# Kernel optimization log

Hardware: AMD Instinct MI355X
Metric: run time of the kernel (lower is better)

Reference implementation:

```python
import jax, jax.numpy as jnp
import numpy as np

N_NODES = 100000
N_EDGES = 1600000
IN_CH = 128
HIDDEN = 64
N_CLASSES = 40


def setup_inputs() -> dict:
    key = jax.random.key(0)
    k_x, k_e, k_w1, k_w2 = jax.random.split(key, 4)
    x = jax.random.normal(k_x, (N_NODES, IN_CH), dtype=jnp.float32)
    edge_index = jax.random.randint(k_e, (2, N_EDGES), 0, N_NODES, dtype=jnp.int64)
    # Glorot-style init for GCN weights
    W1 = jax.random.normal(k_w1, (IN_CH, HIDDEN), dtype=jnp.float32) * (1.0 / np.sqrt(IN_CH))
    b1 = jnp.zeros((HIDDEN,), dtype=jnp.float32)
    W2 = jax.random.normal(k_w2, (HIDDEN, N_CLASSES), dtype=jnp.float32) * (1.0 / np.sqrt(HIDDEN))
    b2 = jnp.zeros((N_CLASSES,), dtype=jnp.float32)
    return {"x": x, "edge_index": edge_index, "W1": W1, "b1": b1, "W2": W2, "b2": b2}


def reference(x, edge_index, W1, b1, W2, b2):
    n = x.shape[0]
    # PyG GCNConv: add self-loops, symmetric degree normalization
    loop = jnp.arange(n, dtype=edge_index.dtype)
    src = jnp.concatenate([edge_index[0], loop])  # message sources j
    dst = jnp.concatenate([edge_index[1], loop])  # aggregation targets i
    w = jnp.ones(src.shape[0], dtype=x.dtype)     # edge_weight=None -> ones
    deg = jax.ops.segment_sum(w, dst, num_segments=n)
    dinv = jnp.where(deg > 0, jax.lax.rsqrt(jnp.maximum(deg, 1e-12)), 0.0)
    norm = dinv[src] * dinv[dst]                  # [E+N]

    def gcn_conv(h, W, b):
        hw = h @ W                                # transform first (fewer flops)
        msg = hw[src] * norm[:, None]             # gather + normalize
        return jax.ops.segment_sum(msg, dst, num_segments=n) + b  # scatter-add

    h = jax.nn.relu(gcn_conv(x, W1, b1))
    # dropout is identity in eval mode
    out = gcn_conv(h, W2, b2)
    return out
```

## Files before the change

### kernel.cpp

```cpp
#include <hip/hip_runtime.h>
#include <hip/hip_bf16.h>

#define NNODES 100000
#define NEDGES 1600000
#define IN_CH 128
#define HID 64
#define NC 40
#define NPAD 100352
#define NBUK 196
#define CAP 9216
#define BCHUNK 4096
#define NBIN 391
#define HW2S 64

typedef unsigned short ushort_t;
typedef unsigned int uint_t;
typedef __attribute__((ext_vector_type(8))) short short8;
typedef __attribute__((ext_vector_type(4))) float floatx4;

__device__ __forceinline__ ushort_t f2bf(float f) {
    union { float ff; unsigned int i; } t;
    t.ff = f;
    unsigned int r = t.i + 0x7fff + ((t.i >> 16) & 1);
    return (ushort_t)(r >> 16);
}
__device__ __forceinline__ float2 unpk(uint_t p) {
    union { unsigned int i; float f; } a, b;
    a.i = p << 16;
    b.i = p & 0xffff0000u;
    return make_float2(a.f, b.f);
}
__device__ __forceinline__ void acc2(float2& a, uint_t p) {
    union { unsigned int i; float f; } lo, hi;
    lo.i = p << 16;
    hi.i = p & 0xffff0000u;
    a.x += lo.f;
    a.y += hi.f;
}

__global__ __launch_bounds__(256) void k_init(
    const float* __restrict__ W1, ushort_t* __restrict__ Wp,
    int* __restrict__ gcur, ushort_t* __restrict__ hw2, int n)
{
    int b = blockIdx.x, t = threadIdx.x;
    if (b < 32) {
        int i = b * 256 + t;
        int j = i & 7;
        int m = (i >> 3) & 15;
        int ct = (i >> 7) & 3;
        int quad = (i >> 9) & 3;
        int kc = i >> 11;
        int k = kc * 32 + quad * 8 + j;
        int c = ct * 16 + m;
        Wp[i] = f2bf(W1[k * HID + c]);
    } else {
        if (t < NBUK) gcur[t] = t * CAP;
        if (t >= 224 && t < 224 + NC) hw2[(size_t)n * HW2S + (t - 224)] = 0;
    }
}

__global__ __launch_bounds__(256) void k_bin0(
    const int* __restrict__ srcs, const int* __restrict__ dsts,
    int* __restrict__ gcur, uint_t* __restrict__ tmp, int e)
{
    __shared__ uint_t pk[BCHUNK];
    __shared__ ushort_t bk[BCHUNK];
    __shared__ int hist[NBUK];
    __shared__ int base[NBUK];
    int t = threadIdx.x;
    int begin = blockIdx.x * BCHUNK;
    int cnt = e - begin; if (cnt > BCHUNK) cnt = BCHUNK;

    for (int i = t; i < NBUK; i += 256) hist[i] = 0;
    __syncthreads();
    for (int j = t; j < cnt; j += 256) {
        int d = dsts[begin + j];
        int s = srcs[begin + j];
        int b = d >> 9;
        pk[j] = (uint_t)s | ((uint_t)(d & 511) << 17);
        bk[j] = (ushort_t)b;
        atomicAdd(&hist[b], 1);
    }
    __syncthreads();
    for (int i = t; i < NBUK; i += 256) {
        base[i] = atomicAdd(&gcur[i], hist[i]);
        hist[i] = 0;
    }
    __syncthreads();
    for (int j = t; j < cnt; j += 256) {
        int b = bk[j];
        int r = atomicAdd(&hist[b], 1);
        int pos = base[b] + r;
        if (pos < (b + 1) * CAP) tmp[pos] = pk[j];
    }
}

__global__ __launch_bounds__(256) void k_sort(
    const uint_t* __restrict__ tmp, const int* __restrict__ gcur,
    int* __restrict__ row_start, float* __restrict__ dinv,
    uint_t* __restrict__ es, int n, int e)
{
    __shared__ int cnt[512];
    __shared__ int sc[512];
    __shared__ int red[256];
    int t = threadIdx.x;
    int b = blockIdx.x;
    int d0 = b << 9;
    int total = gcur[b] - b * CAP;
    if (total > CAP) total = CAP;
    int part = 0;
    for (int i = t; i < b; i += 256) part += gcur[i] - i * CAP;
    red[t] = part;
    cnt[t] = 0; cnt[t + 256] = 0;
    __syncthreads();
    for (int off = 128; off > 0; off >>= 1) {
        if (t < off) red[t] += red[t + off];
        __syncthreads();
    }
    int gb = red[0];
    const uint_t* seg = tmp + b * CAP;
    for (int j = t; j < total; j += 256)
        atomicAdd(&cnt[seg[j] >> 17], 1);
    __syncthreads();
    sc[t] = cnt[t]; sc[t + 256] = cnt[t + 256];
    __syncthreads();
    for (int off = 1; off < 512; off <<= 1) {
        int v0 = (t >= off) ? sc[t - off] : 0;
        int i1 = t + 256;
        int v1 = (i1 >= off) ? sc[i1 - off] : 0;
        __syncthreads();
        sc[t] += v0; sc[i1] += v1;
        __syncthreads();
    }
#pragma unroll
    for (int q = 0; q < 2; ++q) {
        int i = t + q * 256;
        int node = d0 + i;
        int start = gb + sc[i] - cnt[i];
        if (node < n) {
            row_start[node] = start;
            dinv[node] = rsqrtf((float)cnt[i] + 1.0f);
        }
        cnt[i] = start;
    }
    __syncthreads();
    for (int j = t; j < total; j += 256) {
        uint_t p = seg[j];
        int ld = (int)(p >> 17);
        int pos = atomicAdd(&cnt[ld], 1);
        es[pos] = p & 0x1FFFFu;
    }
    if (b == NBUK - 1 && t == 0) row_start[n] = e;
}

__global__ __launch_bounds__(256) void k_gemm1(
    const float* __restrict__ x, const ushort_t* __restrict__ Wp,
    const float* __restrict__ dinv, ushort_t* __restrict__ hw1, int n)
{
    int wave = threadIdx.x >> 6;
    int lane = threadIdx.x & 63;
    int m = lane & 15;
    int quad = lane >> 4;
    int row = blockIdx.x * 64 + wave * 16 + m;
    int rowc = row < n ? row : (n - 1);
    const float* xr = x + (size_t)rowc * IN_CH + quad * 8;

    floatx4 acc[4];
#pragma unroll
    for (int ct = 0; ct < 4; ++ct) acc[ct] = (floatx4){0.f, 0.f, 0.f, 0.f};

#pragma unroll
    for (int kc = 0; kc < 4; ++kc) {
        float4 xa = *(const float4*)(xr + kc * 32);
        float4 xb = *(const float4*)(xr + kc * 32 + 4);
        short8 a;
        a[0] = (short)f2bf(xa.x); a[1] = (short)f2bf(xa.y);
        a[2] = (short)f2bf(xa.z); a[3] = (short)f2bf(xa.w);
        a[4] = (short)f2bf(xb.x); a[5] = (short)f2bf(xb.y);
        a[6] = (short)f2bf(xb.z); a[7] = (short)f2bf(xb.w);
#pragma unroll
        for (int ct = 0; ct < 4; ++ct) {
            short8 b = *(const short8*)(Wp + ((((kc * 4 + quad) * 4 + ct) * 16 + m) << 3));
            acc[ct] = __builtin_amdgcn_mfma_f32_16x16x32_bf16(a, b, acc[ct], 0, 0, 0);
        }
    }
    int r0 = blockIdx.x * 64 + wave * 16 + quad * 4;
#pragma unroll
    for (int r = 0; r < 4; ++r) {
        int rr = r0 + r;
        if (rr < n) {
            float di = dinv[rr];
            ushort_t* o = hw1 + (size_t)rr * HID + m;
#pragma unroll
            for (int ct = 0; ct < 4; ++ct) o[ct * 16] = f2bf(acc[ct][r] * di);
        } else if (rr == n) {
            ushort_t* o = hw1 + (size_t)n * HID + m;
#pragma unroll
            for (int ct = 0; ct < 4; ++ct) o[ct * 16] = 0;
        }
    }
}

__global__ __launch_bounds__(256) void k_agg1(
    const int* __restrict__ row_start, const uint_t* __restrict__ es,
    const float* __restrict__ dinv, const uint_t* __restrict__ hw1u,
    const float* __restrict__ b1, const float* __restrict__ W2,
    ushort_t* __restrict__ hw2, int n)
{
    __shared__ float wsm[HID * NC];
    __shared__ float hsm[32][68];
    for (int i = threadIdx.x; i < HID * NC; i += 256) wsm[i] = W2[i];
    __syncthreads();

    int lane = threadIdx.x & 63;
    int obase = lane & 56;
    int ol = lane & 7;
    int slot = threadIdx.x >> 3;
    int node = blockIdx.x * 32 + slot;
    bool valid = node < n;
    int rs = valid ? row_start[node] : 0;
    int re = valid ? row_start[node + 1] : 0;
    float di = valid ? dinv[node] : 0.f;
    int selfrow = valid ? node : n;

    float2 c0, c1, c2, c3;
    {
        uint4 sp = *(const uint4*)(hw1u + (size_t)selfrow * 32 + ol * 4);
        c0 = unpk(sp.x); c1 = unpk(sp.y); c2 = unpk(sp.z); c3 = unpk(sp.w);
    }
    for (int base = rs; base < re; base += 16) {
        int i0 = base + ol, i1 = base + 8 + ol;
        int elA = (i0 < re) ? (int)es[i0] : n;
        int elB = (i1 < re) ? (int)es[i1] : n;
        int nw = re - base;
        uint4 pA[8], pB[8];
#pragma unroll
        for (int b = 0; b < 8; ++b) {
            int s = __shfl(elA, obase + b);
            pA[b] = *(const uint4*)(hw1u + (size_t)s * 32 + ol * 4);
        }
        bool more = nw > 8;
        if (more) {
#pragma unroll
            for (int b = 0; b < 8; ++b) {
                int s = __shfl(elB, obase + b);
                pB[b] = *(const uint4*)(hw1u + (size_t)s * 32 + ol * 4);
            }
        }
#pragma unroll
        for (int b = 0; b < 8; ++b) {
            acc2(c0, pA[b].x); acc2(c1, pA[b].y);
            acc2(c2, pA[b].z); acc2(c3, pA[b].w);
        }
        if (more) {
#pragma unroll
            for (int b = 0; b < 8; ++b) {
                acc2(c0, pB[b].x); acc2(c1, pB[b].y);
                acc2(c2, pB[b].z); acc2(c3, pB[b].w);
            }
        }
    }
    {
        float4 bb0 = ((const float4*)b1)[ol * 2];
        float4 bb1 = ((const float4*)b1)[ol * 2 + 1];
        float4 h0, h1;
        h0.x = fmaxf(c0.x * di + bb0.x, 0.f);
        h0.y = fmaxf(c0.y * di + bb0.y, 0.f);
        h0.z = fmaxf(c1.x * di + bb0.z, 0.f);
        h0.w = fmaxf(c1.y * di + bb0.w, 0.f);
        h1.x = fmaxf(c2.x * di + bb1.x, 0.f);
        h1.y = fmaxf(c2.y * di + bb1.y, 0.f);
        h1.z = fmaxf(c3.x * di + bb1.z, 0.f);
        h1.w = fmaxf(c3.y * di + bb1.w, 0.f);
        *(float4*)&hsm[slot][ol * 8] = h0;
        *(float4*)&hsm[slot][ol * 8 + 4] = h1;
    }
    int w8 = (threadIdx.x >> 6) * 8;
    int qm = lane >> 4;
    int lq = lane & 15;
    int lw = (lq < 10) ? lq : 0;
    const float4* w4 = (const float4*)wsm;
#pragma unroll
    for (int pass = 0; pass < 2; ++pass) {
        int slot2 = w8 + pass * 4 + qm;
        int node2 = blockIdx.x * 32 + slot2;
        float4 acc = make_float4(0.f, 0.f, 0.f, 0.f);
#pragma unroll 4
        for (int k4 = 0; k4 < 16; ++k4) {
            float4 hk = *(const float4*)&hsm[slot2][k4 * 4];
            float4 w0 = w4[(k4 * 4 + 0) * 10 + lw];
            float4 w1 = w4[(k4 * 4 + 1) * 10 + lw];
            float4 w2 = w4[(k4 * 4 + 2) * 10 + lw];
            float4 w3 = w4[(k4 * 4 + 3) * 10 + lw];
            acc.x += hk.x * w0.x + hk.y * w1.x + hk.z * w2.x + hk.w * w3.x;
            acc.y += hk.x * w0.y + hk.y * w1.y + hk.z * w2.y + hk.w * w3.y;
            acc.z += hk.x * w0.z + hk.y * w1.z + hk.z * w2.z + hk.w * w3.z;
            acc.w += hk.x * w0.w + hk.y * w1.w + hk.z * w2.w + hk.w * w3.w;
        }
        if (node2 < n && lq < 10) {
            float di2 = dinv[node2];
            uint2 st;
            st.x = (uint_t)f2bf(acc.x * di2) | ((uint_t)f2bf(acc.y * di2) << 16);
            st.y = (uint_t)f2bf(acc.z * di2) | ((uint_t)f2bf(acc.w * di2) << 16);
            *(uint2*)(hw2 + (size_t)node2 * HW2S + lq * 4) = st;
        }
    }
}

__global__ __launch_bounds__(256) void k_agg2(
    const int* __restrict__ row_start, const uint_t* __restrict__ es,
    const float* __restrict__ dinv, const uint_t* __restrict__ hw2u,
    const float* __restrict__ b2, float* __restrict__ out, int n)
{
    int lane = threadIdx.x & 63;
    int obase = lane & 56;
    int ol = lane & 7;
    int lc = (ol < 5) ? ol : 0;
    int node = blockIdx.x * 32 + (threadIdx.x >> 3);
    bool valid = node < n;
    int rs = valid ? row_start[node] : 0;
    int re = valid ? row_start[node + 1] : 0;
    float di = valid ? dinv[node] : 0.f;
    int selfrow = valid ? node : n;

    float2 c0, c1, c2, c3;
    {
        uint4 sp = *(const uint4*)(hw2u + (size_t)selfrow * (HW2S / 2) + lc * 4);
        c0 = unpk(sp.x); c1 = unpk(sp.y); c2 = unpk(sp.z); c3 = unpk(sp.w);
    }
    for (int base = rs; base < re; base += 16) {
        int i0 = base + ol, i1 = base + 8 + ol;
        int elA = (i0 < re) ? (int)es[i0] : n;
        int elB = (i1 < re) ? (int)es[i1] : n;
        int nw = re - base;
        uint4 pA[8], pB[8];
#pragma unroll
        for (int b = 0; b < 8; ++b) {
            int s = __shfl(elA, obase + b);
            pA[b] = *(const uint4*)(hw2u + (size_t)s * (HW2S / 2) + lc * 4);
        }
        bool more = nw > 8;
        if (more) {
#pragma unroll
            for (int b = 0; b < 8; ++b) {
                int s = __shfl(elB, obase + b);
                pB[b] = *(const uint4*)(hw2u + (size_t)s * (HW2S / 2) + lc * 4);
            }
        }
#pragma unroll
        for (int b = 0; b < 8; ++b) {
            acc2(c0, pA[b].x); acc2(c1, pA[b].y);
            acc2(c2, pA[b].z); acc2(c3, pA[b].w);
        }
        if (more) {
#pragma unroll
            for (int b = 0; b < 8; ++b) {
                acc2(c0, pB[b].x); acc2(c1, pB[b].y);
                acc2(c2, pB[b].z); acc2(c3, pB[b].w);
            }
        }
    }
    if (valid && ol < 5) {
        float4 bb0 = ((const float4*)b2)[ol * 2];
        float4 bb1 = ((const float4*)b2)[ol * 2 + 1];
        float4 o0, o1;
        o0.x = c0.x * di + bb0.x;
        o0.y = c0.y * di + bb0.y;
        o0.z = c1.x * di + bb0.z;
        o0.w = c1.y * di + bb0.w;
        o1.x = c2.x * di + bb1.x;
        o1.y = c2.y * di + bb1.y;
        o1.z = c3.x * di + bb1.z;
        o1.w = c3.y * di + bb1.w;
        float4* op = (float4*)(out + (size_t)node * 40 + ol * 8);
        op[0] = o0;
        op[1] = o1;
    }
}

extern "C" void kernel_launch(void* const* d_in, const int* in_sizes, int n_in,
                              void* d_out, int out_size, void* d_ws, size_t ws_size,
                              hipStream_t stream) {
    const float* x  = (const float*)d_in[0];
    const int* edge = (const int*)d_in[1];
    const float* W1 = (const float*)d_in[2];
    const float* b1 = (const float*)d_in[3];
    const float* W2 = (const float*)d_in[4];
    const float* b2 = (const float*)d_in[5];
    float* out      = (float*)d_out;

    const int n = in_sizes[0] / IN_CH;
    const int e = in_sizes[1] / 2;
    const int* srcs = edge;
    const int* dsts = edge + e;

    int*      gcur      = (int*)d_ws;
    int*      row_start = gcur + 256;
    float*    dinv      = (float*)(row_start + NPAD);
    uint_t*   tmp       = (uint_t*)(dinv + NPAD);
    uint_t*   es        = tmp + (size_t)NBUK * CAP;
    ushort_t* Wp        = (ushort_t*)(es + NEDGES);
    ushort_t* hw1       = Wp + 8192;
    ushort_t* hw2       = hw1 + (size_t)(NNODES + 1) * HID;

    k_init<<<33, 256, 0, stream>>>(W1, Wp, gcur, hw2, n);
    k_bin0<<<NBIN, 256, 0, stream>>>(srcs, dsts, gcur, tmp, e);
    k_sort<<<NBUK, 256, 0, stream>>>(tmp, gcur, row_start, dinv, es, n, e);
    k_gemm1<<<(n + 63) / 64, 256, 0, stream>>>(x, Wp, dinv, hw1, n);
    k_agg1<<<(n + 31) / 32, 256, 0, stream>>>(row_start, es, dinv, (const uint_t*)hw1, b1, W2, hw2, n);
    k_agg2<<<(n + 31) / 32, 256, 0, stream>>>(row_start, es, dinv, (const uint_t*)hw2, b2, out, n);
}
```

Before: 227.9 us.

## Aggregate layer-2 before W2 transform and add separate fp32 GEMM kernel

Reorders the second GCN layer so it aggregates the 64-wide hidden features first and applies W2 afterwards in a new fp32 GEMM kernel, instead of applying W2 inside the first aggregation. This removes the shared-memory W2 load and per-node matvec from k_agg1, and the gather loops now process 8 neighbours per step instead of 16. In exchange, the second gather reads 64-wide bf16 rows instead of 40-wide ones, an extra fp32 intermediate of 100k×64 is written and read back, and one more kernel is launched.

```diff
diff --git a/kernel.cpp b/kernel.cpp
--- a/kernel.cpp
+++ b/kernel.cpp
@@ -11,7 +11,6 @@
 #define CAP 9216
 #define BCHUNK 4096
 #define NBIN 391
-#define HW2S 64
 
 typedef unsigned short ushort_t;
 typedef unsigned int uint_t;
@@ -40,7 +39,7 @@
 
 __global__ __launch_bounds__(256) void k_init(
     const float* __restrict__ W1, ushort_t* __restrict__ Wp,
-    int* __restrict__ gcur, ushort_t* __restrict__ hw2, int n)
+    int* __restrict__ gcur, ushort_t* __restrict__ hb, int n)
 {
     int b = blockIdx.x, t = threadIdx.x;
     if (b < 32) {
@@ -55,7 +54,8 @@
         Wp[i] = f2bf(W1[k * HID + c]);
     } else {
         if (t < NBUK) gcur[t] = t * CAP;
-        if (t >= 224 && t < 224 + NC) hw2[(size_t)n * HW2S + (t - 224)] = 0;
+        uint_t* hbz = (uint_t*)(hb + (size_t)n * HID);
+        if (t >= 224) hbz[t - 224] = 0;
     }
 }
 
@@ -204,118 +204,11 @@
 __global__ __launch_bounds__(256) void k_agg1(
     const int* __restrict__ row_start, const uint_t* __restrict__ es,
     const float* __restrict__ dinv, const uint_t* __restrict__ hw1u,
-    const float* __restrict__ b1, const float* __restrict__ W2,
-    ushort_t* __restrict__ hw2, int n)
-{
-    __shared__ float wsm[HID * NC];
-    __shared__ float hsm[32][68];
-    for (int i = threadIdx.x; i < HID * NC; i += 256) wsm[i] = W2[i];
-    __syncthreads();
-
+    const float* __restrict__ b1, ushort_t* __restrict__ hb, int n)
+{
     int lane = threadIdx.x & 63;
     int obase = lane & 56;
     int ol = lane & 7;
-    int slot = threadIdx.x >> 3;
-    int node = blockIdx.x * 32 + slot;
-    bool valid = node < n;
-    int rs = valid ? row_start[node] : 0;
-    int re = valid ? row_start[node + 1] : 0;
-    float di = valid ? dinv[node] : 0.f;
-    int selfrow = valid ? node : n;
-
-    float2 c0, c1, c2, c3;
-    {
-        uint4 sp = *(const uint4*)(hw1u + (size_t)selfrow * 32 + ol * 4);
-        c0 = unpk(sp.x); c1 = unpk(sp.y); c2 = unpk(sp.z); c3 = unpk(sp.w);
-    }
-    for (int base = rs; base < re; base += 16) {
-        int i0 = base + ol, i1 = base + 8 + ol;
-        int elA = (i0 < re) ? (int)es[i0] : n;
-        int elB = (i1 < re) ? (int)es[i1] : n;
-        int nw = re - base;
-        uint4 pA[8], pB[8];
-#pragma unroll
-        for (int b = 0; b < 8; ++b) {
-            int s = __shfl(elA, obase + b);
-            pA[b] = *(const uint4*)(hw1u + (size_t)s * 32 + ol * 4);
-        }
-        bool more = nw > 8;
-        if (more) {
-#pragma unroll
-            for (int b = 0; b < 8; ++b) {
-                int s = __shfl(elB, obase + b);
-                pB[b] = *(const uint4*)(hw1u + (size_t)s * 32 + ol * 4);
-            }
-        }
-#pragma unroll
-        for (int b = 0; b < 8; ++b) {
-            acc2(c0, pA[b].x); acc2(c1, pA[b].y);
-            acc2(c2, pA[b].z); acc2(c3, pA[b].w);
-        }
-        if (more) {
-#pragma unroll
-            for (int b = 0; b < 8; ++b) {
-                acc2(c0, pB[b].x); acc2(c1, pB[b].y);
-                acc2(c2, pB[b].z); acc2(c3, pB[b].w);
-            }
-        }
-    }
-    {
-        float4 bb0 = ((const float4*)b1)[ol * 2];
-        float4 bb1 = ((const float4*)b1)[ol * 2 + 1];
-        float4 h0, h1;
-        h0.x = fmaxf(c0.x * di + bb0.x, 0.f);
-        h0.y = fmaxf(c0.y * di + bb0.y, 0.f);
-        h0.z = fmaxf(c1.x * di + bb0.z, 0.f);
-        h0.w = fmaxf(c1.y * di + bb0.w, 0.f);
-        h1.x = fmaxf(c2.x * di + bb1.x, 0.f);
-        h1.y = fmaxf(c2.y * di + bb1.y, 0.f);
-        h1.z = fmaxf(c3.x * di + bb1.z, 0.f);
-        h1.w = fmaxf(c3.y * di + bb1.w, 0.f);
-        *(float4*)&hsm[slot][ol * 8] = h0;
-        *(float4*)&hsm[slot][ol * 8 + 4] = h1;
-    }
-    int w8 = (threadIdx.x >> 6) * 8;
-    int qm = lane >> 4;
-    int lq = lane & 15;
-    int lw = (lq < 10) ? lq : 0;
-    const float4* w4 = (const float4*)wsm;
-#pragma unroll
-    for (int pass = 0; pass < 2; ++pass) {
-        int slot2 = w8 + pass * 4 + qm;
-        int node2 = blockIdx.x * 32 + slot2;
-        float4 acc = make_float4(0.f, 0.f, 0.f, 0.f);
-#pragma unroll 4
-        for (int k4 = 0; k4 < 16; ++k4) {
-            float4 hk = *(const float4*)&hsm[slot2][k4 * 4];
-            float4 w0 = w4[(k4 * 4 + 0) * 10 + lw];
-            float4 w1 = w4[(k4 * 4 + 1) * 10 + lw];
-            float4 w2 = w4[(k4 * 4 + 2) * 10 + lw];
-            float4 w3 = w4[(k4 * 4 + 3) * 10 + lw];
-            acc.x += hk.x * w0.x + hk.y * w1.x + hk.z * w2.x + hk.w * w3.x;
-            acc.y += hk.x * w0.y + hk.y * w1.y + hk.z * w2.y + hk.w * w3.y;
-            acc.z += hk.x * w0.z + hk.y * w1.z + hk.z * w2.z + hk.w * w3.z;
-            acc.w += hk.x * w0.w + hk.y * w1.w + hk.z * w2.w + hk.w * w3.w;
-        }
-        if (node2 < n && lq < 10) {
-            float di2 = dinv[node2];
-            uint2 st;
-            st.x = (uint_t)f2bf(acc.x * di2) | ((uint_t)f2bf(acc.y * di2) << 16);
-            st.y = (uint_t)f2bf(acc.z * di2) | ((uint_t)f2bf(acc.w * di2) << 16);
-            *(uint2*)(hw2 + (size_t)node2 * HW2S + lq * 4) = st;
-        }
-    }
-}
-
-__global__ __launch_bounds__(256) void k_agg2(
-    const int* __restrict__ row_start, const uint_t* __restrict__ es,
-    const float* __restrict__ dinv, const uint_t* __restrict__ hw2u,
-    const float* __restrict__ b2, float* __restrict__ out, int n)
-{
-    int lane = threadIdx.x & 63;
-    int obase = lane & 56;
-    int ol = lane & 7;
-    int lc = (ol < 5) ? ol : 0;
     int node = blockIdx.x * 32 + (threadIdx.x >> 3);
     bool valid = node < n;
     int rs = valid ? row_start[node] : 0;
@@ -325,56 +218,115 @@
 
     float2 c0, c1, c2, c3;
     {
-        uint4 sp = *(const uint4*)(hw2u + (size_t)selfrow * (HW2S / 2) + lc * 4);
+        uint4 sp = *(const uint4*)(hw1u + (size_t)selfrow * 32 + ol * 4);
         c0 = unpk(sp.x); c1 = unpk(sp.y); c2 = unpk(sp.z); c3 = unpk(sp.w);
     }
-    for (int base = rs; base < re; base += 16) {
-        int i0 = base + ol, i1 = base + 8 + ol;
-        int elA = (i0 < re) ? (int)es[i0] : n;
-        int elB = (i1 < re) ? (int)es[i1] : n;
-        int nw = re - base;
-        uint4 pA[8], pB[8];
+    for (int base = rs; base < re; base += 8) {
+        int idx = base + ol;
+        int el = (idx < re) ? (int)es[idx] : n;
+        uint4 p[8];
 #pragma unroll
         for (int b = 0; b < 8; ++b) {
-            int s = __shfl(elA, obase + b);
-            pA[b] = *(const uint4*)(hw2u + (size_t)s * (HW2S / 2) + lc * 4);
-        }
-        bool more = nw > 8;
-        if (more) {
-#pragma unroll
-            for (int b = 0; b < 8; ++b) {
-                int s = __shfl(elB, obase + b);
-                pB[b] = *(const uint4*)(hw2u + (size_t)s * (HW2S / 2) + lc * 4);
-            }
+            int s = __shfl(el, obase + b);
+            p[b] = *(const uint4*)(hw1u + (size_t)s * 32 + ol * 4);
         }
 #pragma unroll
         for (int b = 0; b < 8; ++b) {
-            acc2(c0, pA[b].x); acc2(c1, pA[b].y);
-            acc2(c2, pA[b].z); acc2(c3, pA[b].w);
-        }
-        if (more) {
-#pragma unroll
-            for (int b = 0; b < 8; ++b) {
-                acc2(c0, pB[b].x); acc2(c1, pB[b].y);
-                acc2(c2, pB[b].z); acc2(c3, pB[b].w);
-            }
-        }
-    }
-    if (valid && ol < 5) {
-        float4 bb0 = ((const float4*)b2)[ol * 2];
-        float4 bb1 = ((const float4*)b2)[ol * 2 + 1];
+            acc2(c0, p[b].x); acc2(c1, p[b].y);
+            acc2(c2, p[b].z); acc2(c3, p[b].w);
+        }
+    }
+    if (valid) {
+        float4 bb0 = ((const float4*)b1)[ol * 2];
+        float4 bb1 = ((const float4*)b1)[ol * 2 + 1];
+        float h0 = fmaxf(c0.x * di + bb0.x, 0.f);
+        float h1 = fmaxf(c0.y * di + bb0.y, 0.f);
+        float h2 = fmaxf(c1.x * di + bb0.z, 0.f);
+        float h3 = fmaxf(c1.y * di + bb0.w, 0.f);
+        float h4 = fmaxf(c2.x * di + bb1.x, 0.f);
+        float h5 = fmaxf(c2.y * di + bb1.y, 0.f);
+        float h6 = fmaxf(c3.x * di + bb1.z, 0.f);
+        float h7 = fmaxf(c3.y * di + bb1.w, 0.f);
+        uint4 st;
+        st.x = (uint_t)f2bf(h0 * di) | ((uint_t)f2bf(h1 * di) << 16);
+        st.y = (uint_t)f2bf(h2 * di) | ((uint_t)f2bf(h3 * di) << 16);
+        st.z = (uint_t)f2bf(h4 * di) | ((uint_t)f2bf(h5 * di) << 16);
+        st.w = (uint_t)f2bf(h6 * di) | ((uint_t)f2bf(h7 * di) << 16);
+        *(uint4*)(hb + (size_t)node * HID + ol * 8) = st;
+    }
+}
+
+__global__ __launch_bounds__(256) void k_agg2(
+    const int* __restrict__ row_start, const uint_t* __restrict__ es,
+    const float* __restrict__ dinv, const uint_t* __restrict__ hbu,
+    float* __restrict__ hagg, int n)
+{
+    int lane = threadIdx.x & 63;
+    int obase = lane & 56;
+    int ol = lane & 7;
+    int node = blockIdx.x * 32 + (threadIdx.x >> 3);
+    bool valid = node < n;
+    int rs = valid ? row_start[node] : 0;
+    int re = valid ? row_start[node + 1] : 0;
+    float di = valid ? dinv[node] : 0.f;
+    int selfrow = valid ? node : n;
+
+    float2 c0, c1, c2, c3;
+    {
+        uint4 sp = *(const uint4*)(hbu + (size_t)selfrow * 32 + ol * 4);
+        c0 = unpk(sp.x); c1 = unpk(sp.y); c2 = unpk(sp.z); c3 = unpk(sp.w);
+    }
+    for (int base = rs; base < re; base += 8) {
+        int idx = base + ol;
+        int el = (idx < re) ? (int)es[idx] : n;
+        uint4 p[8];
+#pragma unroll
+        for (int b = 0; b < 8; ++b) {
+            int s = __shfl(el, obase + b);
+            p[b] = *(const uint4*)(hbu + (size_t)s * 32 + ol * 4);
+        }
+#pragma unroll
+        for (int b = 0; b < 8; ++b) {
+            acc2(c0, p[b].x); acc2(c1, p[b].y);
+            acc2(c2, p[b].z); acc2(c3, p[b].w);
+        }
+    }
+    if (valid) {
         float4 o0, o1;
-        o0.x = c0.x * di + bb0.x;
-        o0.y = c0.y * di + bb0.y;
-        o0.z = c1.x * di + bb0.z;
-        o0.w = c1.y * di + bb0.w;
-        o1.x = c2.x * di + bb1.x;
-        o1.y = c2.y * di + bb1.y;
-        o1.z = c3.x * di + bb1.z;
-        o1.w = c3.y * di + bb1.w;
-        float4* op = (float4*)(out + (size_t)node * 40 + ol * 8);
-        op[0] = o0;
-        op[1] = o1;
+        o0.x = c0.x * di; o0.y = c0.y * di; o0.z = c1.x * di; o0.w = c1.y * di;
+        o1.x = c2.x * di; o1.y = c2.y * di; o1.z = c3.x * di; o1.w = c3.y * di;
+        float* hr = hagg + (size_t)node * HID + ol * 8;
+        *(float4*)hr = o0;
+        *(float4*)(hr + 4) = o1;
+    }
+}
+
+__global__ __launch_bounds__(256) void k_gemm2f(
+    const float* __restrict__ hagg, const float* __restrict__ W2,
+    const float* __restrict__ b2, float* __restrict__ out, int n)
+{
+    __shared__ float wsm[HID * NC];
+    for (int i = threadIdx.x; i < HID * NC; i += 256) wsm[i] = W2[i];
+    __syncthreads();
+    int row = blockIdx.x * 256 + threadIdx.x;
+    if (row >= n) return;
+    const float4* hr = (const float4*)(hagg + (size_t)row * HID);
+    float acc[NC];
+#pragma unroll
+    for (int c = 0; c < NC; ++c) acc[c] = b2[c];
+#pragma unroll 4
+    for (int k4 = 0; k4 < HID / 4; ++k4) {
+        float4 hv = hr[k4];
+        const float* w0 = wsm + (k4 * 4) * NC;
+#pragma unroll
+        for (int c = 0; c < NC; ++c)
+            acc[c] += hv.x * w0[c] + hv.y * w0[c + NC] + hv.z * w0[c + 2 * NC] + hv.w * w0[c + 3 * NC];
+    }
+    float* o = out + (size_t)row * NC;
+#pragma unroll
+    for (int c4 = 0; c4 < NC / 4; ++c4) {
+        float4 st = make_float4(acc[4 * c4], acc[4 * c4 + 1], acc[4 * c4 + 2], acc[4 * c4 + 3]);
+        *(float4*)(o + 4 * c4) = st;
     }
 }
 
@@ -401,12 +353,14 @@
     uint_t*   es        = tmp + (size_t)NBUK * CAP;
     ushort_t* Wp        = (ushort_t*)(es + NEDGES);
     ushort_t* hw1       = Wp + 8192;
-    ushort_t* hw2       = hw1 + (size_t)(NNODES + 1) * HID;
-
-    k_init<<<33, 256, 0, stream>>>(W1, Wp, gcur, hw2, n);
+    ushort_t* hb        = hw1 + (size_t)(NNODES + 1) * HID;
+    float*    hagg      = (float*)(hb + (size_t)(NNODES + 1) * HID);
+
+    k_init<<<33, 256, 0, stream>>>(W1, Wp, gcur, hb, n);
     k_bin0<<<NBIN, 256, 0, stream>>>(srcs, dsts, gcur, tmp, e);
     k_sort<<<NBUK, 256, 0, stream>>>(tmp, gcur, row_start, dinv, es, n, e);
     k_gemm1<<<(n + 63) / 64, 256, 0, stream>>>(x, Wp, dinv, hw1, n);
-    k_agg1<<<(n + 31) / 32, 256, 0, stream>>>(row_start, es, dinv, (const uint_t*)hw1, b1, W2, hw2, n);
-    k_agg2<<<(n + 31) / 32, 256, 0, stream>>>(row_start, es, dinv, (const uint_t*)hw2, b2, out, n);
-}
+    k_agg1<<<(n + 31) / 32, 256, 0, stream>>>(row_start, es, dinv, (const uint_t*)hw1, b1, hb, n);
+    k_agg2<<<(n + 31) / 32, 256, 0, stream>>>(row_start, es, dinv, (const uint_t*)hb, hagg, n);
+    k_gemm2f<<<(n + 255) / 256, 256, 0, stream>>>(hagg, W2, b2, out, n);
+}
```

Result: slower. 238.1 us (+4.5%).
